# Optimization experiments

Measured on AMD Instinct MI355X. Metric: run time of the kernel, lower is better.

Reference implementation:

```python
import jax, jax.numpy as jnp
import numpy as np
import math

B, N, D, H = 4, 2048, 256, 4
DH = D // H
EPS = 1e-8


def setup_inputs() -> dict:
    key = jax.random.key(0)
    ks = jax.random.split(key, 8)
    x = jax.random.normal(ks[0], (B, N, D), dtype=jnp.float32)
    # RoPE rotation freqs: exp(i * pos * inv_freq), stored as (cos, sin) pairs -> [N, DH//2, 2]
    d2 = DH // 2
    inv_freq = 1.0 / (10000.0 ** (jnp.arange(d2, dtype=jnp.float32) / d2))
    ang = jnp.arange(N, dtype=jnp.float32)[:, None] * inv_freq[None, :]
    freqs = jnp.stack([jnp.cos(ang), jnp.sin(ang)], axis=-1)  # [N, d2, 2]
    s = 0.02
    g = jnp.ones((D,), dtype=jnp.float32)
    w_qkv = jax.random.normal(ks[1], (D, 3 * D), dtype=jnp.float32) * s
    b_qkv = jnp.zeros((3 * D,), dtype=jnp.float32)
    w_out = jax.random.normal(ks[2], (D, D), dtype=jnp.float32) * s
    b_out = jnp.zeros((D,), dtype=jnp.float32)
    w_gate = jax.random.normal(ks[3], (D, D), dtype=jnp.float32) * s
    b_gate = jnp.zeros((D,), dtype=jnp.float32)
    return {"x": x, "freqs": freqs, "g": g, "w_qkv": w_qkv, "b_qkv": b_qkv,
            "w_out": w_out, "b_out": b_out, "w_gate": w_gate, "b_gate": b_gate}


def _zcrmsnorm(x, g):
    x0 = x - jnp.mean(x, axis=-1, keepdims=True)
    rms = jnp.sqrt(jnp.mean(x0 * x0, axis=-1, keepdims=True) + EPS)
    return x0 / rms * g


def _rope(q, freqs):
    # q: [B,H,N,DH]; freqs: [N,DH//2,2] (cos,sin). Complex multiply on adjacent pairs.
    b, h, n, dh = q.shape
    qp = q.reshape(b, h, n, dh // 2, 2)
    cos = freqs[:n, :, 0][None, None]  # [1,1,N,d2]
    sin = freqs[:n, :, 1][None, None]
    q0, q1 = qp[..., 0], qp[..., 1]
    out = jnp.stack([q0 * cos - q1 * sin, q0 * sin + q1 * cos], axis=-1)
    return out.reshape(b, h, n, dh)


def reference(x, freqs, g, w_qkv, b_qkv, w_out, b_out, w_gate, b_gate):
    b, n, d = x.shape
    h = _zcrmsnorm(x, g)
    qkv = (h @ w_qkv + b_qkv).reshape(b, n, 3, H, DH)
    qkv = jnp.transpose(qkv, (2, 0, 3, 1, 4))  # [3,B,H,N,DH]
    q, k, v = qkv[0], qkv[1], qkv[2]
    q = _rope(q, freqs)
    k = _rope(k, freqs)
    scores = jnp.einsum('bhqd,bhkd->bhqk', q, k) / math.sqrt(DH)
    attn = jax.nn.softmax(scores, axis=-1)  # dropout is identity in eval
    y = jnp.einsum('bhqk,bhkd->bhqd', attn, v)
    y = jnp.transpose(y, (0, 2, 1, 3)).reshape(b, n, d)
    y = y @ w_out + b_out
    gate = jax.nn.sigmoid(h @ w_gate + b_gate)
    return x + gate * y
```

## Files before the change

### kernel.cpp

```cpp
#include <hip/hip_runtime.h>

typedef unsigned short u16;
typedef unsigned int u32;
typedef short short8 __attribute__((ext_vector_type(8)));
typedef float f32x4 __attribute__((ext_vector_type(4)));

#define B_ 4
#define N_ 2048
#define D_ 256
#define H_ 4
#define DH_ 64
#define BN_ 8192

__device__ inline float b2f(u16 u) {
    union { u32 i; float f; } v; v.i = ((u32)u) << 16; return v.f;
}
__device__ inline u16 f2b(float f) {
    union { float f; u32 i; } v; v.f = f;
    return (u16)((v.i + 0x8000u) >> 16);
}
__device__ inline u32 pkbf(float a, float b) {
    union { float f; u32 i; } ua, ub; ua.f = a; ub.f = b;
    return __builtin_amdgcn_perm(ub.i + 0x8000u, ua.i + 0x8000u, 0x07060302u);
}
__device__ inline f32x4 mfma16(short8 a, short8 b, f32x4 c) {
    return __builtin_amdgcn_mfma_f32_16x16x32_bf16(a, b, c, 0, 0, 0);
}

__device__ __forceinline__ void gemm_body(
    int bx, int by, int tid,
    const u16* __restrict__ A, const u16* __restrict__ BT,
    const float* __restrict__ bias, void* __restrict__ Cout,
    int Ntot)
{
    const int wave = tid >> 6, lane = tid & 63;
    const int ln15 = lane & 15, quad = lane >> 4;
    const int m0 = bx * 128 + (wave & 1) * 64;
    const int n0 = by * 128 + (wave >> 1) * 64;

    const f32x4 zero = {0.f, 0.f, 0.f, 0.f};
    f32x4 acc[4][4];
    #pragma unroll
    for (int i = 0; i < 4; ++i)
        #pragma unroll
        for (int j = 0; j < 4; ++j) acc[i][j] = zero;

    #pragma unroll
    for (int k0 = 0; k0 < 256; k0 += 32) {
        const int koff = k0 + quad * 8;
        short8 a[4], b[4];
        #pragma unroll
        for (int i = 0; i < 4; ++i)
            a[i] = *(const short8*)(A + (size_t)(m0 + i * 16 + ln15) * 256 + koff);
        #pragma unroll
        for (int j = 0; j < 4; ++j)
            b[j] = *(const short8*)(BT + (size_t)(n0 + j * 16 + ln15) * 256 + koff);
        #pragma unroll
        for (int i = 0; i < 4; ++i)
            #pragma unroll
            for (int j = 0; j < 4; ++j)
                acc[i][j] = mfma16(a[i], b[j], acc[i][j]);
    }

    #pragma unroll
    for (int i = 0; i < 4; ++i) {
        const int r = m0 + i * 16 + quad * 4;
        #pragma unroll
        for (int j = 0; j < 4; ++j) {
            const int c = n0 + j * 16 + ln15;
            const float bv = bias[c];
            #pragma unroll
            for (int rg = 0; rg < 4; ++rg) {
                const size_t idx = (size_t)(r + rg) * Ntot + c;
                ((u16*)Cout)[idx] = f2b(acc[i][j][rg] + bv);
            }
        }
    }
}

__device__ __forceinline__ void gemm_thin_body(
    int bx, int by, int tid,
    const u16* __restrict__ A, const u16* __restrict__ BT,
    const float* __restrict__ bias, void* __restrict__ Cout,
    const float* __restrict__ xin, const u16* __restrict__ gate,
    int mode)
{
    const int wave = tid >> 6, lane = tid & 63;
    const int ln15 = lane & 15, quad = lane >> 4;
    const int m0 = bx * 64 + (wave & 1) * 32;
    const int n0 = by * 64 + (wave >> 1) * 32;

    const f32x4 zero = {0.f, 0.f, 0.f, 0.f};
    f32x4 acc[2][2];
    #pragma unroll
    for (int i = 0; i < 2; ++i)
        #pragma unroll
        for (int j = 0; j < 2; ++j) acc[i][j] = zero;

    #pragma unroll
    for (int k0 = 0; k0 < 256; k0 += 32) {
        const int koff = k0 + quad * 8;
        short8 a[2], b[2];
        #pragma unroll
        for (int i = 0; i < 2; ++i)
            a[i] = *(const short8*)(A + (size_t)(m0 + i * 16 + ln15) * 256 + koff);
        #pragma unroll
        for (int j = 0; j < 2; ++j)
            b[j] = *(const short8*)(BT + (size_t)(n0 + j * 16 + ln15) * 256 + koff);
        #pragma unroll
        for (int i = 0; i < 2; ++i)
            #pragma unroll
            for (int j = 0; j < 2; ++j)
                acc[i][j] = mfma16(a[i], b[j], acc[i][j]);
    }

    #pragma unroll
    for (int i = 0; i < 2; ++i) {
        const int r = m0 + i * 16 + quad * 4;
        #pragma unroll
        for (int j = 0; j < 2; ++j) {
            const int c = n0 + j * 16 + ln15;
            const float bv = bias[c];
            #pragma unroll
            for (int rg = 0; rg < 4; ++rg) {
                const size_t idx = (size_t)(r + rg) * 256 + c;
                float v = acc[i][j][rg] + bv;
                if (mode == 1) {
                    ((u16*)Cout)[idx] = f2b(1.0f / (1.0f + __expf(-v)));
                } else {
                    ((float*)Cout)[idx] = xin[idx] + b2f(gate[idx]) * v;
                }
            }
        }
    }
}

__global__ __launch_bounds__(256) void gemm_ep(
    const u16* __restrict__ A, const u16* __restrict__ BT,
    const float* __restrict__ bias, void* __restrict__ Cout, int Ntot)
{
    gemm_body(blockIdx.x, blockIdx.y, threadIdx.x, A, BT, bias, Cout, Ntot);
}

__global__ __launch_bounds__(256) void gemm_thin(
    const u16* __restrict__ A, const u16* __restrict__ BT,
    const float* __restrict__ bias, void* __restrict__ Cout,
    const float* __restrict__ xin, const u16* __restrict__ gate, int mode)
{
    gemm_thin_body(blockIdx.x, blockIdx.y, threadIdx.x, A, BT, bias, Cout,
                   xin, gate, mode);
}

__global__ __launch_bounds__(256) void norm_transw_k(
    const float* __restrict__ x, const float* __restrict__ g, u16* __restrict__ h,
    const float* __restrict__ wqkv, const float* __restrict__ wout,
    const float* __restrict__ wgate,
    u16* __restrict__ wqkvT, u16* __restrict__ woutT, u16* __restrict__ wgateT)
{
    if (blockIdx.x < 2048) {
        const int wave = threadIdx.x >> 6, lane = threadIdx.x & 63;
        const int t = blockIdx.x * 4 + wave;
        const float4 u = *(const float4*)(x + (size_t)t * D_ + lane * 4);
        float s  = u.x + u.y + u.z + u.w;
        float s2 = u.x * u.x + u.y * u.y + u.z * u.z + u.w * u.w;
        #pragma unroll
        for (int m = 1; m < 64; m <<= 1) {
            s  += __shfl_xor(s, m);
            s2 += __shfl_xor(s2, m);
        }
        float mean = s * (1.0f / D_);
        float var  = s2 * (1.0f / D_) - mean * mean;
        float rinv = rsqrtf(var + 1e-8f);
        const float4 gv = *(const float4*)(g + lane * 4);
        uint2 o;
        o.x = pkbf((u.x - mean) * rinv * gv.x, (u.y - mean) * rinv * gv.y);
        o.y = pkbf((u.z - mean) * rinv * gv.z, (u.w - mean) * rinv * gv.w);
        *(uint2*)(h + (size_t)t * D_ + lane * 4) = o;
    } else {
        int idx = (blockIdx.x - 2048) * 256 + threadIdx.x;
        if (idx < 768 * 256) {
            int nn = idx >> 8, kk = idx & 255;
            wqkvT[idx] = f2b(wqkv[kk * 768 + nn]);
        }
        idx -= 768 * 256;
        if (idx >= 0 && idx < 256 * 256) {
            int nn = idx >> 8, kk = idx & 255;
            woutT[idx]  = f2b(wout[kk * 256 + nn]);
            wgateT[idx] = f2b(wgate[kk * 256 + nn]);
        }
    }
}

#define QSCALE 0.18033688f
__global__ __launch_bounds__(256) void rope_vt_gate_k(
    const u16* __restrict__ qkv, const float* __restrict__ freqs,
    u16* __restrict__ Q, u16* __restrict__ K, u16* __restrict__ VT,
    const u16* __restrict__ h, const u16* __restrict__ wgateT,
    const float* __restrict__ b_gate, u16* __restrict__ gatb)
{
    __shared__ __align__(16) u16 tile[64 * 65];
    const int blk = blockIdx.x;
    if (blk < 1024) {
        const int idx = blk * 256 + threadIdx.x;
        const int t = idx >> 5, rem = idx & 31;
        const int hh = rem >> 3, s8 = rem & 7;
        const int b = t >> 11, n = t & 2047;

        const float4 f0 = *(const float4*)(freqs + (size_t)n * 64 + s8 * 8);
        const float4 f1 = *(const float4*)(freqs + (size_t)n * 64 + s8 * 8 + 4);

        const u16* qp = qkv + (size_t)t * 768 + hh * 64 + s8 * 8;
        const uint4 qv = *(const uint4*)qp;
        const uint4 kv = *(const uint4*)(qp + 256);

        const size_t off = ((size_t)(b * H_ + hh) * N_ + n) * DH_ + s8 * 8;
        uint4 qo, ko;
        {
            float q0 = b2f((u16)(qv.x & 0xffff)), q1 = b2f((u16)(qv.x >> 16));
            float k0 = b2f((u16)(kv.x & 0xffff)), k1 = b2f((u16)(kv.x >> 16));
            qo.x = pkbf((q0 * f0.x - q1 * f0.y) * QSCALE, (q0 * f0.y + q1 * f0.x) * QSCALE);
            ko.x = pkbf(k0 * f0.x - k1 * f0.y, k0 * f0.y + k1 * f0.x);
        }
        {
            float q0 = b2f((u16)(qv.y & 0xffff)), q1 = b2f((u16)(qv.y >> 16));
            float k0 = b2f((u16)(kv.y & 0xffff)), k1 = b2f((u16)(kv.y >> 16));
            qo.y = pkbf((q0 * f0.z - q1 * f0.w) * QSCALE, (q0 * f0.w + q1 * f0.z) * QSCALE);
            ko.y = pkbf(k0 * f0.z - k1 * f0.w, k0 * f0.w + k1 * f0.z);
        }
        {
            float q0 = b2f((u16)(qv.z & 0xffff)), q1 = b2f((u16)(qv.z >> 16));
            float k0 = b2f((u16)(kv.z & 0xffff)), k1 = b2f((u16)(kv.z >> 16));
            qo.z = pkbf((q0 * f1.x - q1 * f1.y) * QSCALE, (q0 * f1.y + q1 * f1.x) * QSCALE);
            ko.z = pkbf(k0 * f1.x - k1 * f1.y, k0 * f1.y + k1 * f1.x);
        }
        {
            float q0 = b2f((u16)(qv.w & 0xffff)), q1 = b2f((u16)(qv.w >> 16));
            float k0 = b2f((u16)(kv.w & 0xffff)), k1 = b2f((u16)(kv.w >> 16));
            qo.w = pkbf((q0 * f1.z - q1 * f1.w) * QSCALE, (q0 * f1.w + q1 * f1.z) * QSCALE);
            ko.w = pkbf(k0 * f1.z - k1 * f1.w, k0 * f1.w + k1 * f1.z);
        }
        *(uint4*)(Q + off) = qo;
        *(uint4*)(K + off) = ko;
    } else if (blk < 1536) {
        const int id2 = blk - 1024;
        const int bh = id2 & 15;
        const int n0 = (id2 >> 4) * 64;
        const int b = bh >> 2, hh = bh & 3;
        #pragma unroll
        for (int rep = 0; rep < 16; ++rep) {
            int idx = rep * 256 + threadIdx.x;
            int nl = idx >> 6, dh = idx & 63;
            tile[dh * 65 + nl] = qkv[(size_t)(b * N_ + n0 + nl) * 768 + 512 + hh * 64 + dh];
        }
        __syncthreads();
        #pragma unroll
        for (int rep = 0; rep < 16; ++rep) {
            int idx = rep * 256 + threadIdx.x;
            int dh = idx >> 6, nl = idx & 63;
            VT[((size_t)bh * 64 + dh) * N_ + n0 + nl] = tile[dh * 65 + nl];
        }
    } else {
        const int id3 = blk - 1536;
        gemm_thin_body(id3 & 127, id3 >> 7, threadIdx.x, h, wgateT, b_gate,
                       (void*)gatb, (const float*)nullptr, (const u16*)nullptr, 1);
    }
}

__global__ __launch_bounds__(256) void attn_k(
    const u16* __restrict__ Q, const u16* __restrict__ K,
    const u16* __restrict__ VT, u16* __restrict__ yt)
{
    __shared__ __align__(16) u16 Ks[2][64][72];
    __shared__ __align__(16) u16 Vs[2][64][72];
    __shared__ __align__(16) u16 Pb[4][16 * 88];
    const int tid = threadIdx.x;
    const int wave = tid >> 6, lane = tid & 63;
    const int ln15 = lane & 15, quad = lane >> 4;
    const int id = blockIdx.x;
    const int bh = ((id & 7) << 1) | ((id >> 3) & 1);
    const int q0 = (id >> 4) * 64 + wave * 16;

    const u16* Qh = Q + (size_t)bh * N_ * DH_;
    const u16* Kh = K + (size_t)bh * N_ * DH_;
    const u16* Vh = VT + (size_t)bh * DH_ * N_;

    const short8 bq0 = *(const short8*)(Qh + (size_t)(q0 + ln15) * DH_ + quad * 8);
    const short8 bq1 = *(const short8*)(Qh + (size_t)(q0 + ln15) * DH_ + 32 + quad * 8);

    const f32x4 zero = {0.f, 0.f, 0.f, 0.f};
    f32x4 o[4];
    #pragma unroll
    for (int j = 0; j < 4; ++j) o[j] = zero;
    float lv = 0.f;
    u16* Pw = Pb[wave];

    const int srow = tid >> 2, sq4 = tid & 3;

    {
        uint4 k0 = *(const uint4*)(Kh + (size_t)srow * DH_ + sq4 * 8);
        uint4 k1 = *(const uint4*)(Kh + (size_t)srow * DH_ + (sq4 + 4) * 8);
        uint4 v0 = *(const uint4*)(Vh + (size_t)srow * N_ + sq4 * 8);
        uint4 v1 = *(const uint4*)(Vh + (size_t)srow * N_ + (sq4 + 4) * 8);
        *(uint4*)&Ks[0][srow][sq4 * 8] = k0;
        *(uint4*)&Ks[0][srow][(sq4 + 4) * 8] = k1;
        *(uint4*)&Vs[0][srow][sq4 * 8] = v0;
        *(uint4*)&Vs[0][srow][(sq4 + 4) * 8] = v1;
    }
    __syncthreads();

    int p = 0;
    for (int c = 0; c < 32; ++c) {
        const int ktn = (c + 1) * 64;
        uint4 k0, k1, v0, v1;
        const bool more = (c + 1 < 32);
        if (more) {
            k0 = *(const uint4*)(Kh + (size_t)(ktn + srow) * DH_ + sq4 * 8);
            k1 = *(const uint4*)(Kh + (size_t)(ktn + srow) * DH_ + (sq4 + 4) * 8);
            v0 = *(const uint4*)(Vh + (size_t)srow * N_ + ktn + sq4 * 8);
            v1 = *(const uint4*)(Vh + (size_t)srow * N_ + ktn + (sq4 + 4) * 8);
        }

        f32x4 st[4];
        #pragma unroll
        for (int c4 = 0; c4 < 4; ++c4) {
            short8 ka0 = *(const short8*)&Ks[p][c4 * 16 + ln15][quad * 8];
            short8 ka1 = *(const short8*)&Ks[p][c4 * 16 + ln15][32 + quad * 8];
            st[c4] = mfma16(ka0, bq0, zero);
            st[c4] = mfma16(ka1, bq1, st[c4]);
        }
        f32x4 pr[4];
        float rs = 0.f;
        #pragma unroll
        for (int c4 = 0; c4 < 4; ++c4) {
            #pragma unroll
            for (int r = 0; r < 4; ++r) {
                pr[c4][r] = exp2f(st[c4][r]);
                rs += pr[c4][r];
            }
        }
        lv += rs;
        #pragma unroll
        for (int c4 = 0; c4 < 4; ++c4) {
            uint2 w;
            w.x = pkbf(pr[c4][0], pr[c4][1]);
            w.y = pkbf(pr[c4][2], pr[c4][3]);
            *(uint2*)(Pw + ln15 * 88 + c4 * 16 + quad * 4) = w;
        }
        asm volatile("s_waitcnt lgkmcnt(0)" ::: "memory");
        const short8 bp0 = *(const short8*)(Pw + ln15 * 88 + quad * 8);
        const short8 bp1 = *(const short8*)(Pw + ln15 * 88 + 32 + quad * 8);
        #pragma unroll
        for (int j = 0; j < 4; ++j) {
            short8 va0 = *(const short8*)&Vs[p][j * 16 + ln15][quad * 8];
            short8 va1 = *(const short8*)&Vs[p][j * 16 + ln15][32 + quad * 8];
            o[j] = mfma16(va0, bp0, o[j]);
            o[j] = mfma16(va1, bp1, o[j]);
        }

        if (more) {
            *(uint4*)&Ks[p ^ 1][srow][sq4 * 8] = k0;
            *(uint4*)&Ks[p ^ 1][srow][(sq4 + 4) * 8] = k1;
            *(uint4*)&Vs[p ^ 1][srow][sq4 * 8] = v0;
            *(uint4*)&Vs[p ^ 1][srow][(sq4 + 4) * 8] = v1;
        }
        __syncthreads();
        p ^= 1;
    }

    lv += __shfl_xor(lv, 16);
    lv += __shfl_xor(lv, 32);
    const float rl = 1.0f / lv;
    const int b = bh >> 2, h = bh & 3;
    const size_t base = ((size_t)b * N_ + q0 + ln15) * D_ + h * 64;
    #pragma unroll
    for (int j = 0; j < 4; ++j) {
        uint2 w;
        w.x = pkbf(o[j][0] * rl, o[j][1] * rl);
        w.y = pkbf(o[j][2] * rl, o[j][3] * rl);
        *(uint2*)(yt + base + j * 16 + quad * 4) = w;
    }
}

extern "C" void kernel_launch(void* const* d_in, const int* in_sizes, int n_in,
                              void* d_out, int out_size, void* d_ws, size_t ws_size,
                              hipStream_t stream) {
    const float* x      = (const float*)d_in[0];
    const float* freqs  = (const float*)d_in[1];
    const float* g      = (const float*)d_in[2];
    const float* w_qkv  = (const float*)d_in[3];
    const float* b_qkv  = (const float*)d_in[4];
    const float* w_out  = (const float*)d_in[5];
    const float* b_out  = (const float*)d_in[6];
    const float* w_gate = (const float*)d_in[7];
    const float* b_gate = (const float*)d_in[8];
    float* out = (float*)d_out;

    char* ws = (char*)d_ws;
    size_t off = 0;
    auto carve = [&](size_t nelem) -> u16* {
        u16* p = (u16*)(ws + off);
        off += ((nelem * 2 + 255) / 256) * 256;
        return p;
    };
    u16* h      = carve((size_t)BN_ * D_);
    u16* qkv    = carve((size_t)BN_ * 768);
    u16* Qb     = carve((size_t)BN_ * D_);
    u16* Kb     = carve((size_t)BN_ * D_);
    u16* VT     = carve((size_t)BN_ * D_);
    u16* gatb   = carve((size_t)BN_ * D_);
    u16* wqkvT  = carve((size_t)768 * 256);
    u16* woutT  = carve((size_t)256 * 256);
    u16* wgateT = carve((size_t)256 * 256);
    u16* yt = qkv;

    hipLaunchKernelGGL(norm_transw_k, dim3(3072), dim3(256), 0, stream,
                       x, g, h, w_qkv, w_out, w_gate, wqkvT, woutT, wgateT);
    hipLaunchKernelGGL(gemm_ep, dim3(BN_ / 128, 6), dim3(256), 0, stream,
                       h, wqkvT, b_qkv, (void*)qkv, 768);
    hipLaunchKernelGGL(rope_vt_gate_k, dim3(2048), dim3(256), 0, stream,
                       qkv, freqs, Qb, Kb, VT, h, wgateT, b_gate, gatb);
    hipLaunchKernelGGL(attn_k, dim3(512), dim3(256), 0, stream,
                       Qb, Kb, VT, yt);
    hipLaunchKernelGGL(gemm_thin, dim3(128, 4), dim3(256), 0, stream,
                       yt, woutT, b_out, (void*)out, x, gatb, 2);
}
```

Measured before the change: 168.2 us.

## Load K/V fragments directly from global into registers, drop LDS staging

The attention kernel no longer stages K and V tiles through double-buffered shared memory. Each wave now loads its MFMA operand fragments straight from global memory into registers, prefetching the next K chunk while computing the current one. A raw s_barrier is kept at the end of each iteration, and launch bounds now ask for two blocks per CU. This removes the LDS write/read traffic and the block-wide synchronisation, but each of the four waves re-reads the same K/V data from global memory or L2, quadrupling load traffic and relying on the cache.

```diff
diff --git a/kernel.cpp b/kernel.cpp
--- a/kernel.cpp
+++ b/kernel.cpp
@@ -266,12 +266,10 @@
     }
 }
 
-__global__ __launch_bounds__(256) void attn_k(
+__global__ __launch_bounds__(256, 2) void attn_k(
     const u16* __restrict__ Q, const u16* __restrict__ K,
     const u16* __restrict__ VT, u16* __restrict__ yt)
 {
-    __shared__ __align__(16) u16 Ks[2][64][72];
-    __shared__ __align__(16) u16 Vs[2][64][72];
     __shared__ __align__(16) u16 Pb[4][16 * 88];
     const int tid = threadIdx.x;
     const int wave = tid >> 6, lane = tid & 63;
@@ -287,6 +285,9 @@
     const short8 bq0 = *(const short8*)(Qh + (size_t)(q0 + ln15) * DH_ + quad * 8);
     const short8 bq1 = *(const short8*)(Qh + (size_t)(q0 + ln15) * DH_ + 32 + quad * 8);
 
+    const u16* kbase = Kh + (size_t)ln15 * DH_ + quad * 8;
+    const u16* vbase = Vh + (size_t)ln15 * N_ + quad * 8;
+
     const f32x4 zero = {0.f, 0.f, 0.f, 0.f};
     f32x4 o[4];
     #pragma unroll
@@ -294,40 +295,38 @@
     float lv = 0.f;
     u16* Pw = Pb[wave];
 
-    const int srow = tid >> 2, sq4 = tid & 3;
-
-    {
-        uint4 k0 = *(const uint4*)(Kh + (size_t)srow * DH_ + sq4 * 8);
-        uint4 k1 = *(const uint4*)(Kh + (size_t)srow * DH_ + (sq4 + 4) * 8);
-        uint4 v0 = *(const uint4*)(Vh + (size_t)srow * N_ + sq4 * 8);
-        uint4 v1 = *(const uint4*)(Vh + (size_t)srow * N_ + (sq4 + 4) * 8);
-        *(uint4*)&Ks[0][srow][sq4 * 8] = k0;
-        *(uint4*)&Ks[0][srow][(sq4 + 4) * 8] = k1;
-        *(uint4*)&Vs[0][srow][sq4 * 8] = v0;
-        *(uint4*)&Vs[0][srow][(sq4 + 4) * 8] = v1;
-    }
-    __syncthreads();
-
-    int p = 0;
+    short8 ka[8];
+    #pragma unroll
+    for (int c4 = 0; c4 < 4; ++c4) {
+        ka[c4 * 2]     = *(const short8*)(kbase + (size_t)c4 * 16 * DH_);
+        ka[c4 * 2 + 1] = *(const short8*)(kbase + (size_t)c4 * 16 * DH_ + 32);
+    }
+
     for (int c = 0; c < 32; ++c) {
-        const int ktn = (c + 1) * 64;
-        uint4 k0, k1, v0, v1;
-        const bool more = (c + 1 < 32);
-        if (more) {
-            k0 = *(const uint4*)(Kh + (size_t)(ktn + srow) * DH_ + sq4 * 8);
-            k1 = *(const uint4*)(Kh + (size_t)(ktn + srow) * DH_ + (sq4 + 4) * 8);
-            v0 = *(const uint4*)(Vh + (size_t)srow * N_ + ktn + sq4 * 8);
-            v1 = *(const uint4*)(Vh + (size_t)srow * N_ + ktn + (sq4 + 4) * 8);
+        short8 va[8];
+        #pragma unroll
+        for (int j = 0; j < 4; ++j) {
+            const u16* vp = vbase + (size_t)j * 16 * N_ + c * 64;
+            va[j * 2]     = *(const short8*)vp;
+            va[j * 2 + 1] = *(const short8*)(vp + 32);
         }
 
         f32x4 st[4];
         #pragma unroll
         for (int c4 = 0; c4 < 4; ++c4) {
-            short8 ka0 = *(const short8*)&Ks[p][c4 * 16 + ln15][quad * 8];
-            short8 ka1 = *(const short8*)&Ks[p][c4 * 16 + ln15][32 + quad * 8];
-            st[c4] = mfma16(ka0, bq0, zero);
-            st[c4] = mfma16(ka1, bq1, st[c4]);
-        }
+            st[c4] = mfma16(ka[c4 * 2], bq0, zero);
+            st[c4] = mfma16(ka[c4 * 2 + 1], bq1, st[c4]);
+        }
+
+        if (c + 1 < 32) {
+            const u16* kp = kbase + (size_t)(c + 1) * 64 * DH_;
+            #pragma unroll
+            for (int c4 = 0; c4 < 4; ++c4) {
+                ka[c4 * 2]     = *(const short8*)(kp + (size_t)c4 * 16 * DH_);
+                ka[c4 * 2 + 1] = *(const short8*)(kp + (size_t)c4 * 16 * DH_ + 32);
+            }
+        }
+
         f32x4 pr[4];
         float rs = 0.f;
         #pragma unroll
@@ -339,6 +338,7 @@
             }
         }
         lv += rs;
+
         #pragma unroll
         for (int c4 = 0; c4 < 4; ++c4) {
             uint2 w;
@@ -349,22 +349,14 @@
         asm volatile("s_waitcnt lgkmcnt(0)" ::: "memory");
         const short8 bp0 = *(const short8*)(Pw + ln15 * 88 + quad * 8);
         const short8 bp1 = *(const short8*)(Pw + ln15 * 88 + 32 + quad * 8);
+
         #pragma unroll
         for (int j = 0; j < 4; ++j) {
-            short8 va0 = *(const short8*)&Vs[p][j * 16 + ln15][quad * 8];
-            short8 va1 = *(const short8*)&Vs[p][j * 16 + ln15][32 + quad * 8];
-            o[j] = mfma16(va0, bp0, o[j]);
-            o[j] = mfma16(va1, bp1, o[j]);
-        }
-
-        if (more) {
-            *(uint4*)&Ks[p ^ 1][srow][sq4 * 8] = k0;
-            *(uint4*)&Ks[p ^ 1][srow][(sq4 + 4) * 8] = k1;
-            *(uint4*)&Vs[p ^ 1][srow][sq4 * 8] = v0;
-            *(uint4*)&Vs[p ^ 1][srow][(sq4 + 4) * 8] = v1;
-        }
-        __syncthreads();
-        p ^= 1;
+            o[j] = mfma16(va[j * 2], bp0, o[j]);
+            o[j] = mfma16(va[j * 2 + 1], bp1, o[j]);
+        }
+
+        __builtin_amdgcn_s_barrier();
     }
 
     lv += __shfl_xor(lv, 16);
```

New measurement: 242.4 us. 1.44x slower.
